# Performance work log

Hardware: AMD Instinct MI355X
Metric: run time of the kernel (lower is better)

## Reference

```python
import jax, jax.numpy as jnp
import numpy as np

EPS = 1e-5

def masked_group_norm(x, mask, gamma, beta, num_groups):
    # x: [B,D,H,W,C] (zero at unoccupied), mask: [B,D,H,W,1] float
    B, D, H, W, C = x.shape
    G = num_groups
    Cg = C // G
    xg = x.reshape(B, -1, G, Cg)          # [B,V,G,Cg]
    m = mask.reshape(B, -1, 1, 1)         # [B,V,1,1]
    cnt = jnp.maximum(m.sum(axis=1, keepdims=True) * Cg, 1.0)  # elems per (B,G)
    mean = (xg * m).sum(axis=(1, 3), keepdims=True) / cnt
    var = (((xg - mean) ** 2) * m).sum(axis=(1, 3), keepdims=True) / cnt
    y = (xg - mean) * jax.lax.rsqrt(var + EPS)
    y = y.reshape(B, D, H, W, C)
    return (y * gamma + beta) * mask

def downsample2(x, mask):
    # mean-pool occupied children under coords//2; new site occupied if any child is
    B, D, H, W, C = x.shape
    xr = x.reshape(B, D // 2, 2, H // 2, 2, W // 2, 2, C)
    mr = mask.reshape(B, D // 2, 2, H // 2, 2, W // 2, 2, 1)
    cnt = mr.sum(axis=(2, 4, 6))
    y = xr.sum(axis=(2, 4, 6)) / jnp.maximum(cnt, 1.0)
    new_mask = (cnt > 0).astype(x.dtype)
    return y, new_mask

def subm_conv3d(x, w, b, mask):
    # submanifold conv: unoccupied inputs are zero; outputs only at occupied sites
    y = jax.lax.conv_general_dilated(
        x, w, window_strides=(1, 1, 1), padding='SAME',
        dimension_numbers=('NDHWC', 'DHWIO', 'NDHWC'))
    return (y + b) * mask

def setup_inputs() -> dict:
    key = jax.random.key(0)
    ks = jax.random.split(key, 12)
    B, D, C, Co = 4, 64, 64, 128
    x = jax.random.normal(ks[0], (B, D, D, D, C), dtype=jnp.float32)
    mask = jax.random.randint(ks[1], (B, D, D, D), 0, 2).astype(jnp.int32)
    s = 0.05
    return {
        'x': x, 'mask': mask,
        'gn1_w': jnp.ones((C,), jnp.float32), 'gn1_b': jnp.zeros((C,), jnp.float32),
        'w1': jax.random.normal(ks[2], (3, 3, 3, C, Co), jnp.float32) * s,
        'b1': jax.random.normal(ks[3], (Co,), jnp.float32) * s,
        'gn2_w': jnp.ones((Co,), jnp.float32), 'gn2_b': jnp.zeros((Co,), jnp.float32),
        'w2': jax.random.normal(ks[4], (3, 3, 3, Co, Co), jnp.float32) * s,
        'b2': jax.random.normal(ks[5], (Co,), jnp.float32) * s,
        'wskip': jax.random.normal(ks[6], (C, Co), jnp.float32) * s,
        'bskip': jax.random.normal(ks[7], (Co,), jnp.float32) * s,
    }

def reference(x, mask, gn1_w, gn1_b, w1, b1, gn2_w, gn2_b, w2, b2, wskip, bskip):
    NUM_GROUPS = 32
    m = mask.astype(x.dtype)[..., None]          # [B,D,H,W,1]
    x = x * m                                    # sparse tensor: zero off-mask
    # act_layers: SparseGroupNorm32 + SparseSiLU
    h = masked_group_norm(x, m, gn1_w, gn1_b, NUM_GROUPS)
    h = jax.nn.silu(h)                           # silu(0)=0, stays sparse
    # downsample both h and residual x
    h, dm = downsample2(h, m)
    xd, _ = downsample2(x, m)
    # out_layers: conv3 -> GN -> SiLU -> conv3
    h = subm_conv3d(h, w1, b1, dm)
    h = masked_group_norm(h, dm, gn2_w, gn2_b, NUM_GROUPS)
    h = jax.nn.silu(h)
    h = subm_conv3d(h, w2, b2, dm)
    # skip: 1x1 sparse conv (out_channels != channels)
    skip = (jnp.einsum('bdhwc,co->bdhwo', xd, wskip) + bskip) * dm
    return h + skip
```

## Files before the change

### kernel.cpp

```cpp
#include <hip/hip_runtime.h>
#include <cstdint>
#include <cstddef>

#define B_ 4
#define V1 262144
#define C1 64
#define V2 32768
#define C2 128
#define TOTV 131072
#define P_ 34
#define P2_ 1156
#define P3_ 39304
#define SBSTRIDE ((size_t)4 * P3_)

#define OFF_S1A 0
#define OFF_S2A 128
#define OFF_CNT1 256
#define OFF_S1B 260
#define OFF_S2B 388
#define OFF_CNT2 516

typedef __bf16 bf16x8 __attribute__((ext_vector_type(8)));
typedef float f32x4 __attribute__((ext_vector_type(4)));

__device__ __forceinline__ float bf2f(unsigned short u) {
    return __builtin_bit_cast(float, (unsigned)u << 16);
}
__device__ __forceinline__ unsigned short f2bf(float f) {
    unsigned u = __builtin_bit_cast(unsigned, f);
    u += 0x7fffu + ((u >> 16) & 1u);
    return (unsigned short)(u >> 16);
}

__device__ __forceinline__ int a_ofs(int ks, int csh) {
    int s = ks & ((1 << csh) - 1), tap = ks >> csh;
    int dz = tap / 9, r = tap % 9, dy = r / 3, dx = r % 3;
    return s * (int)(SBSTRIDE * 64) + (dz * P2_ + dy * P_ + dx) * 64;
}

__global__ __launch_bounds__(256) void k0_wprep(const float* __restrict__ w1,
                                                const float* __restrict__ w2,
                                                const float* __restrict__ wskip,
                                                unsigned short* __restrict__ w1t,
                                                unsigned short* __restrict__ w2t,
                                                int* __restrict__ d1,
                                                int* __restrict__ d2)
{
    int i = blockIdx.x * 256 + threadIdx.x;
    if (blockIdx.x == 0) {
        int t = threadIdx.x;
        if (t < 54)               d1[t] = (t + 1 < 54)  ? a_ofs(t + 1, 1) - a_ofs(t, 1) : 0;
        if (t >= 64 && t < 172) { int j = t - 64;
                                  d2[j] = (j + 1 < 108) ? a_ofs(j + 1, 2) - a_ofs(j, 2) : 0; }
    }
    if (i < 54 * 4096) {
        int slab = i >> 12, r = i & 4095;
        int q = r >> 10, n = (r >> 3) & 127, j = r & 7;
        int t = slab >> 1, s = slab & 1;
        int ci = s * 32 + q * 8 + j;
        w1t[i] = f2bf(w1[((size_t)t * 64 + ci) * 128 + n]);
    }
    int i2 = i - 54 * 4096;
    if (i2 >= 0 && i2 < 110 * 4096) {
        int slab = i2 >> 12, r = i2 & 4095;
        int q = r >> 10, n = (r >> 3) & 127, j = r & 7;
        float v;
        if (slab < 108) {
            int t = slab >> 2, s = slab & 3;
            int ci = s * 32 + q * 8 + j;
            v = w2[((size_t)t * 128 + ci) * 128 + n];
        } else {
            int ci = (slab - 108) * 32 + q * 8 + j;
            v = wskip[(size_t)ci * 128 + n];
        }
        w2t[i2] = f2bf(v);
    }
}

__global__ __launch_bounds__(256) void kz_border(unsigned short* __restrict__ h1p,
                                                 unsigned short* __restrict__ h2p)
{
    int i = blockIdx.x * 256 + threadIdx.x;
    if (i >= 24 * P3_) return;
    int sb = i / P3_, vox = i % P3_;
    int vz = vox / P2_, r = vox % P2_, vy = r / P_, vx = r % P_;
    bool border = (vz == 0) | (vz == 33) | (vy == 0) | (vy == 33) | (vx == 0) | (vx == 33);
    if (!border) return;
    unsigned short* base = (sb < 8) ? (h1p + (size_t)sb * P3_ * 32 + (size_t)vox * 32)
                                    : (h2p + (size_t)(sb - 8) * P3_ * 32 + (size_t)vox * 32);
    uint4 z = {0, 0, 0, 0};
    uint4* b4 = (uint4*)base;
    b4[0] = z; b4[1] = z; b4[2] = z; b4[3] = z;
}

__global__ __launch_bounds__(256) void k1_stats1(const float* __restrict__ x,
                                                 const int* __restrict__ mask,
                                                 float* __restrict__ stats)
{
    __shared__ float ls1[32], ls2[32];
    __shared__ float lcnt;
    int tid = threadIdx.x;
    if (tid < 32) { ls1[tid] = 0.f; ls2[tid] = 0.f; }
    if (tid == 0) lcnt = 0.f;
    __syncthreads();

    int b  = blockIdx.x & 3;
    int bb = blockIdx.x >> 2;
    int c4 = tid & 15;
    int vl = tid >> 4;

    const float* xb = x + ((size_t)b * V1) * C1;
    const int*   mb = mask + (size_t)b * V1;

    float s1a = 0.f, s2a = 0.f, s1b = 0.f, s2b = 0.f, mc = 0.f;
    for (int ch = bb; ch < V1 / 16; ch += 1024) {
        int v = ch * 16 + vl;
        int m = mb[v];
        if (c4 == 0) mc += (float)m;
        if (m) {
            float4 xv = *(const float4*)(xb + (size_t)v * C1 + c4 * 4);
            s1a += xv.x + xv.y;  s2a += xv.x * xv.x + xv.y * xv.y;
            s1b += xv.z + xv.w;  s2b += xv.z * xv.z + xv.w * xv.w;
        }
    }
    atomicAdd(&ls1[2 * c4],     s1a); atomicAdd(&ls2[2 * c4],     s2a);
    atomicAdd(&ls1[2 * c4 + 1], s1b); atomicAdd(&ls2[2 * c4 + 1], s2b);
    if (c4 == 0) atomicAdd(&lcnt, mc);
    __syncthreads();
    if (tid < 32) {
        atomicAdd(&stats[OFF_S1A + b * 32 + tid], ls1[tid]);
        atomicAdd(&stats[OFF_S2A + b * 32 + tid], ls2[tid]);
    }
    if (tid == 0) atomicAdd(&stats[OFF_CNT1 + b], lcnt);
}

__global__ __launch_bounds__(256) void k2_down(const float* __restrict__ x,
                                               const int* __restrict__ mask,
                                               const float* __restrict__ gn1w,
                                               const float* __restrict__ gn1b,
                                               const float* __restrict__ stats,
                                               unsigned short* __restrict__ h1p,
                                               unsigned short* __restrict__ xdb,
                                               float* __restrict__ dm)
{
    int tid = threadIdx.x;
    int c  = tid & 63;
    int vl = tid >> 6;
    size_t ov = (size_t)blockIdx.x * 4 + vl;
    int b  = (int)(ov >> 15);
    int v2 = (int)(ov & 32767);
    int z = v2 >> 10, y = (v2 >> 5) & 31, xk = v2 & 31;

    int g = c >> 1;
    float ce   = fmaxf(stats[OFF_CNT1 + b] * 2.f, 1.f);
    float mean = stats[OFF_S1A + b * 32 + g] / ce;
    float var  = stats[OFF_S2A + b * 32 + g] / ce - mean * mean;
    float rinv = rsqrtf(var + 1e-5f);
    float a  = rinv * gn1w[c];
    float bc = gn1b[c] - mean * a;

    const int*   mb = mask + ((size_t)b << 18);
    const float* xb = x + (((size_t)b << 18) << 6);

    float hacc = 0.f, xacc = 0.f; int cnt = 0;
    #pragma unroll
    for (int dz = 0; dz < 2; ++dz)
    #pragma unroll
    for (int dy = 0; dy < 2; ++dy)
    #pragma unroll
    for (int dx = 0; dx < 2; ++dx) {
        int v1 = ((2 * z + dz) << 12) | ((2 * y + dy) << 6) | (2 * xk + dx);
        if (mb[v1]) {
            cnt++;
            float xv = xb[(size_t)v1 * 64 + c];
            xacc += xv;
            float yv = fmaf(xv, a, bc);
            hacc += yv / (1.f + expf(-yv));
        }
    }
    float inv = 1.f / fmaxf((float)cnt, 1.f);
    int pvox = (z + 1) * P2_ + (y + 1) * P_ + (xk + 1);
    size_t so = ((size_t)(c >> 5) * SBSTRIDE + (size_t)b * P3_ + pvox) * 32 + (c & 31);
    h1p[so] = f2bf(hacc * inv);
    xdb[ov * 64 + c] = f2bf(xacc * inv);
    if (c == 0) dm[ov] = (cnt > 0) ? 1.f : 0.f;
}

template<int CIN, bool SKIP>
__global__ __launch_bounds__(256, 4) void conv3_mfma(
    const unsigned short* __restrict__ srcP,
    const unsigned short* __restrict__ sksrc,
    const unsigned short* __restrict__ wT,
    const int* __restrict__ tblA,
    const float* __restrict__ bias,
    const float* __restrict__ bias2,
    const float* __restrict__ dm,
    float* __restrict__ outf,
    unsigned short* __restrict__ outb)
{
    constexpr int CS   = CIN / 32;
    constexpr int NKM  = 27 * CS;
    constexpr int NPHM = NKM / 2;
    constexpr int NPH  = NPHM + (SKIP ? 1 : 0);

    __shared__ short smem[2][8192];

    const int tid  = threadIdx.x;
    const int lane = tid & 63;
    const int wv   = tid >> 6;
    const int orig = blockIdx.x;
    const int blk  = (orig & 7) * 128 + (orig >> 3);
    const int b    = blk >> 8;
    const int z    = (blk >> 3) & 31;
    const int yo   = blk & 7;
    const int y0   = yo * 4 + wv;
    const int vb   = b * 32768;
    const int klo  = (lane >> 4) * 8;
    const int xl   = lane & 15;
    const int rlo  = (lane >> 4) * 4;

    f32x4 acc[2][8];
    #pragma unroll
    for (int f = 0; f < 2; ++f)
        #pragma unroll
        for (int nb = 0; nb < 8; ++nb)
            acc[f][nb] = (f32x4){0.f, 0.f, 0.f, 0.f};

    const char* pA = (const char*)srcP +
        (((size_t)b * P3_ + (size_t)(z * P2_ + y0 * P_ + xl)) * 32 + klo) * 2;

    auto loadSkip = [&](int ss, bf16x8* af) {
        const unsigned short* abase = sksrc + ss * 32;
        #pragma unroll
        for (int f = 0; f < 2; ++f) {
            int xx = f * 16 + xl;
            af[f] = *(const bf16x8*)(abase +
                     (size_t)(vb + z * 1024 + y0 * 32 + xx) * 64 + klo);
        }
    };

    auto stageW = [&](int pr, int buf) {
        const char* g = (const char*)wT + (size_t)pr * 16384 + wv * 1024 + (lane << 4);
        char* l = (char*)&smem[0][0] + buf * 16384 + wv * 1024;
        #pragma unroll
        for (int j = 0; j < 4; ++j)
            __builtin_amdgcn_global_load_lds(
                (const __attribute__((address_space(1))) unsigned int*)(g + j * 4096),
                (__attribute__((address_space(3))) unsigned int*)(l + j * 4096),
                16, 0, 0);
    };

    bf16x8 afc[4];
    stageW(0, 0);
    afc[0] = *(const bf16x8*)pA; afc[1] = *(const bf16x8*)(pA + 1024); pA += tblA[0];
    afc[2] = *(const bf16x8*)pA; afc[3] = *(const bf16x8*)(pA + 1024); pA += tblA[1];
    asm volatile("s_waitcnt vmcnt(4)" ::: "memory");
    __builtin_amdgcn_s_barrier();

    int cur = 0;
    #pragma unroll 2
    for (int p = 0; p < NPH; ++p) {
        const bool more = (p + 1 < NPH);
        bf16x8 afn[4] = {{}, {}, {}, {}};
        if (more) {
            stageW(p + 1, cur ^ 1);
            if (2 * p + 2 < NKM) {
                afn[0] = *(const bf16x8*)pA; afn[1] = *(const bf16x8*)(pA + 1024);
                pA += tblA[2 * p + 2];
                afn[2] = *(const bf16x8*)pA; afn[3] = *(const bf16x8*)(pA + 1024);
                pA += tblA[2 * p + 3];
            } else if (SKIP) {
                loadSkip(0, &afn[0]);
                loadSkip(1, &afn[2]);
            }
        }
        __builtin_amdgcn_s_setprio(1);
        #pragma unroll
        for (int ss = 0; ss < 2; ++ss) {
            const short* bp = &smem[0][0] + cur * 8192 + ss * 4096 +
                              ((lane >> 4) * 128 + xl) * 8;
            #pragma unroll
            for (int nb = 0; nb < 8; ++nb) {
                bf16x8 bfr = *(const bf16x8*)(bp + nb * 128);
                acc[0][nb] = __builtin_amdgcn_mfma_f32_16x16x32_bf16(afc[ss * 2 + 0], bfr, acc[0][nb], 0, 0, 0);
                acc[1][nb] = __builtin_amdgcn_mfma_f32_16x16x32_bf16(afc[ss * 2 + 1], bfr, acc[1][nb], 0, 0, 0);
            }
        }
        __builtin_amdgcn_s_setprio(0);
        if (more) asm volatile("s_waitcnt vmcnt(4)" ::: "memory");
        else      asm volatile("s_waitcnt vmcnt(0)" ::: "memory");
        asm volatile("s_waitcnt lgkmcnt(0)" ::: "memory");
        __builtin_amdgcn_s_barrier();
        afc[0] = afn[0]; afc[1] = afn[1]; afc[2] = afn[2]; afc[3] = afn[3];
        cur ^= 1;
    }

    float bv[8];
    #pragma unroll
    for (int nb = 0; nb < 8; ++nb) {
        int co = nb * 16 + xl;
        if constexpr (SKIP) bv[nb] = bias[co] + bias2[co];
        else                bv[nb] = bias[co];
    }
    #pragma unroll
    for (int f = 0; f < 2; ++f) {
        int xb2 = f * 16 + rlo;
        #pragma unroll
        for (int j = 0; j < 4; ++j) {
            int vox = vb + z * 1024 + y0 * 32 + xb2 + j;
            float dmx = dm[vox];
            #pragma unroll
            for (int nb = 0; nb < 8; ++nb) {
                float o = (acc[f][nb][j] + bv[nb]) * dmx;
                if constexpr (SKIP) outf[(size_t)vox * 128 + nb * 16 + xl] = o;
                else                outb[(size_t)vox * 128 + nb * 16 + xl] = f2bf(o);
            }
        }
    }
}

__global__ __launch_bounds__(256) void k4_stats2(const unsigned short* __restrict__ h2a,
                                                 const float* __restrict__ dm,
                                                 float* __restrict__ stats)
{
    __shared__ float ls1[32], ls2[32];
    __shared__ float lcnt;
    int tid = threadIdx.x;
    if (tid < 32) { ls1[tid] = 0.f; ls2[tid] = 0.f; }
    if (tid == 0) lcnt = 0.f;
    __syncthreads();

    int b  = blockIdx.x & 3;
    int bb = blockIdx.x >> 2;
    int g  = tid & 31;
    int vl = tid >> 5;

    const unsigned short* hb = h2a + ((size_t)b * V2) * C2;
    const float* dmb = dm + (size_t)b * V2;

    float s1 = 0.f, s2 = 0.f, mc = 0.f;
    for (int ch = bb; ch < V2 / 8; ch += 1024) {
        int v = ch * 8 + vl;
        float m = dmb[v];
        if (g == 0) mc += m;
        if (m != 0.f) {
            ushort4 hv = *(const ushort4*)(hb + (size_t)v * C2 + g * 4);
            float h0 = bf2f(hv.x), h1 = bf2f(hv.y), h2 = bf2f(hv.z), h3 = bf2f(hv.w);
            s1 += h0 + h1 + h2 + h3;
            s2 += h0 * h0 + h1 * h1 + h2 * h2 + h3 * h3;
        }
    }
    atomicAdd(&ls1[g], s1); atomicAdd(&ls2[g], s2);
    if (g == 0) atomicAdd(&lcnt, mc);
    __syncthreads();
    if (tid < 32) {
        atomicAdd(&stats[OFF_S1B + b * 32 + tid], ls1[tid]);
        atomicAdd(&stats[OFF_S2B + b * 32 + tid], ls2[tid]);
    }
    if (tid == 0) atomicAdd(&stats[OFF_CNT2 + b], lcnt);
}

__global__ __launch_bounds__(256) void k5_gn2(const unsigned short* __restrict__ h2a,
                                              unsigned short* __restrict__ h2p,
                                              const float* __restrict__ stats,
                                              const float* __restrict__ dm,
                                              const float* __restrict__ gn2w,
                                              const float* __restrict__ gn2b)
{
    int idx = blockIdx.x * 256 + threadIdx.x;
    int v = idx >> 5, g = idx & 31;
    int b = v >> 15;
    int v2 = v & 32767;
    float ce   = fmaxf(stats[OFF_CNT2 + b] * 4.f, 1.f);
    float mean = stats[OFF_S1B + b * 32 + g] / ce;
    float var  = stats[OFF_S2B + b * 32 + g] / ce - mean * mean;
    float rinv = rsqrtf(var + 1e-5f);
    float dmv  = dm[v];
    ushort4 hv = *(const ushort4*)(h2a + (size_t)idx * 4);
    float4 gw = *(const float4*)(gn2w + g * 4);
    float4 gb = *(const float4*)(gn2b + g * 4);
    float a, t;
    ushort4 o;
    a = rinv * gw.x; t = (fmaf(bf2f(hv.x), a, gb.x - mean * a)) * dmv; o.x = f2bf(t / (1.f + expf(-t)));
    a = rinv * gw.y; t = (fmaf(bf2f(hv.y), a, gb.y - mean * a)) * dmv; o.y = f2bf(t / (1.f + expf(-t)));
    a = rinv * gw.z; t = (fmaf(bf2f(hv.z), a, gb.z - mean * a)) * dmv; o.z = f2bf(t / (1.f + expf(-t)));
    a = rinv * gw.w; t = (fmaf(bf2f(hv.w), a, gb.w - mean * a)) * dmv; o.w = f2bf(t / (1.f + expf(-t)));
    int zz = v2 >> 10, yy = (v2 >> 5) & 31, xx = v2 & 31;
    int pvox = (zz + 1) * P2_ + (yy + 1) * P_ + (xx + 1);
    size_t so = ((size_t)(g >> 3) * SBSTRIDE + (size_t)b * P3_ + pvox) * 32 + (g & 7) * 4;
    *(ushort4*)(h2p + so) = o;
}

extern "C" void kernel_launch(void* const* d_in, const int* in_sizes, int n_in,
                              void* d_out, int out_size, void* d_ws, size_t ws_size,
                              hipStream_t stream)
{
    const float* x     = (const float*)d_in[0];
    const int*   mask  = (const int*)d_in[1];
    const float* gn1w  = (const float*)d_in[2];
    const float* gn1b  = (const float*)d_in[3];
    const float* w1    = (const float*)d_in[4];
    const float* b1    = (const float*)d_in[5];
    const float* gn2w  = (const float*)d_in[6];
    const float* gn2b  = (const float*)d_in[7];
    const float* w2    = (const float*)d_in[8];
    const float* b2    = (const float*)d_in[9];
    const float* wskip = (const float*)d_in[10];
    const float* bskip = (const float*)d_in[11];
    float* out = (float*)d_out;

    char* wsb = (char*)d_ws;
    float*          stats = (float*)wsb;
    float*          dm    = (float*)(wsb + 4096);
    unsigned short* h1p   = (unsigned short*)(wsb + 528384);
    unsigned short* xdb   = (unsigned short*)(wsb + 20652032);
    unsigned short* h2a   = (unsigned short*)(wsb + 37429248);
    unsigned short* h2p   = (unsigned short*)(wsb + 70983680);
    unsigned short* w1t   = (unsigned short*)(wsb + 111230976);
    unsigned short* w2t   = (unsigned short*)(wsb + 111673344);
    int*            d1    = (int*)(wsb + 112574464);
    int*            d2    = (int*)(wsb + 112574720);

    hipMemsetAsync(stats, 0, 520 * sizeof(float), stream);

    hipLaunchKernelGGL(k0_wprep, dim3(2624), dim3(256), 0, stream, w1, w2, wskip, w1t, w2t, d1, d2);
    hipLaunchKernelGGL(kz_border, dim3((24 * P3_ + 255) / 256), dim3(256), 0, stream, h1p, h2p);
    hipLaunchKernelGGL(k1_stats1, dim3(4096), dim3(256), 0, stream, x, mask, stats);
    hipLaunchKernelGGL(k2_down, dim3(32768), dim3(256), 0, stream,
                       x, mask, gn1w, gn1b, stats, h1p, xdb, dm);
    hipLaunchKernelGGL((conv3_mfma<64, false>), dim3(1024), dim3(256), 0, stream,
                       h1p, (const unsigned short*)nullptr, w1t, d1, b1, (const float*)nullptr,
                       dm, (float*)nullptr, h2a);
    hipLaunchKernelGGL(k4_stats2, dim3(4096), dim3(256), 0, stream, h2a, dm, stats);
    hipLaunchKernelGGL(k5_gn2, dim3(16384), dim3(256), 0, stream, h2a, h2p, stats, dm, gn2w, gn2b);
    hipLaunchKernelGGL((conv3_mfma<128, true>), dim3(1024), dim3(256), 0, stream,
                       h2p, xdb, w2t, d2, b2, bskip, dm, out, (unsigned short*)nullptr);
}
```

Baseline: 442.1 us.

## Double per-wave output tile in conv MFMA kernels to reuse weight fragments

Each wave now computes two y-rows (64 voxels) instead of one, holding 4x8 accumulators. Each LDS weight fragment then feeds four MFMAs instead of two, which halves LDS weight traffic and weight staging per output. The grid is halved to 512 blocks and launch bounds drop to 2 blocks per CU. In exchange, register pressure and A-fragment loads per step double, and occupancy falls, with only 512 blocks to spread over the GPU's CUs. The dm epilogue now loads four mask values at once with a float4.

```diff
diff --git a/kernel.cpp b/kernel.cpp
--- a/kernel.cpp
+++ b/kernel.cpp
@@ -187,7 +187,7 @@
 }
 
 template<int CIN, bool SKIP>
-__global__ __launch_bounds__(256, 4) void conv3_mfma(
+__global__ __launch_bounds__(256, 2) void conv3_mfma(
     const unsigned short* __restrict__ srcP,
     const unsigned short* __restrict__ sksrc,
     const unsigned short* __restrict__ wT,
@@ -209,19 +209,19 @@
     const int lane = tid & 63;
     const int wv   = tid >> 6;
     const int orig = blockIdx.x;
-    const int blk  = (orig & 7) * 128 + (orig >> 3);
-    const int b    = blk >> 8;
-    const int z    = (blk >> 3) & 31;
-    const int yo   = blk & 7;
-    const int y0   = yo * 4 + wv;
+    const int blk  = (orig & 7) * 64 + (orig >> 3);
+    const int b    = blk >> 7;
+    const int z    = (blk >> 2) & 31;
+    const int yo   = blk & 3;
+    const int y0   = yo * 8 + wv * 2;
     const int vb   = b * 32768;
     const int klo  = (lane >> 4) * 8;
     const int xl   = lane & 15;
     const int rlo  = (lane >> 4) * 4;
 
-    f32x4 acc[2][8];
-    #pragma unroll
-    for (int f = 0; f < 2; ++f)
+    f32x4 acc[4][8];
+    #pragma unroll
+    for (int f = 0; f < 4; ++f)
         #pragma unroll
         for (int nb = 0; nb < 8; ++nb)
             acc[f][nb] = (f32x4){0.f, 0.f, 0.f, 0.f};
@@ -232,11 +232,11 @@
     auto loadSkip = [&](int ss, bf16x8* af) {
         const unsigned short* abase = sksrc + ss * 32;
         #pragma unroll
-        for (int f = 0; f < 2; ++f) {
-            int xx = f * 16 + xl;
-            af[f] = *(const bf16x8*)(abase +
-                     (size_t)(vb + z * 1024 + y0 * 32 + xx) * 64 + klo);
-        }
+        for (int fy = 0; fy < 2; ++fy)
+            #pragma unroll
+            for (int fx = 0; fx < 2; ++fx)
+                af[fy * 2 + fx] = *(const bf16x8*)(abase +
+                    (size_t)(vb + z * 1024 + (y0 + fy) * 32 + fx * 16 + xl) * 64 + klo);
     };
 
     auto stageW = [&](int pr, int buf) {
@@ -250,28 +250,34 @@
                 16, 0, 0);
     };
 
-    bf16x8 afc[4];
+    auto loadAStep = [&](int ks, bf16x8* af) {
+        af[0] = *(const bf16x8*)pA;
+        af[1] = *(const bf16x8*)(pA + 1024);
+        af[2] = *(const bf16x8*)(pA + 2176);
+        af[3] = *(const bf16x8*)(pA + 3200);
+        pA += tblA[ks];
+    };
+
+    bf16x8 afc[8];
     stageW(0, 0);
-    afc[0] = *(const bf16x8*)pA; afc[1] = *(const bf16x8*)(pA + 1024); pA += tblA[0];
-    afc[2] = *(const bf16x8*)pA; afc[3] = *(const bf16x8*)(pA + 1024); pA += tblA[1];
-    asm volatile("s_waitcnt vmcnt(4)" ::: "memory");
+    loadAStep(0, &afc[0]);
+    loadAStep(1, &afc[4]);
+    asm volatile("s_waitcnt vmcnt(8)" ::: "memory");
     __builtin_amdgcn_s_barrier();
 
     int cur = 0;
     #pragma unroll 2
     for (int p = 0; p < NPH; ++p) {
         const bool more = (p + 1 < NPH);
-        bf16x8 afn[4] = {{}, {}, {}, {}};
+        bf16x8 afn[8] = {{}, {}, {}, {}, {}, {}, {}, {}};
         if (more) {
             stageW(p + 1, cur ^ 1);
             if (2 * p + 2 < NKM) {
-                afn[0] = *(const bf16x8*)pA; afn[1] = *(const bf16x8*)(pA + 1024);
-                pA += tblA[2 * p + 2];
-                afn[2] = *(const bf16x8*)pA; afn[3] = *(const bf16x8*)(pA + 1024);
-                pA += tblA[2 * p + 3];
+                loadAStep(2 * p + 2, &afn[0]);
+                loadAStep(2 * p + 3, &afn[4]);
             } else if (SKIP) {
                 loadSkip(0, &afn[0]);
-                loadSkip(1, &afn[2]);
+                loadSkip(1, &afn[4]);
             }
         }
         __builtin_amdgcn_s_setprio(1);
@@ -282,16 +288,19 @@
             #pragma unroll
             for (int nb = 0; nb < 8; ++nb) {
                 bf16x8 bfr = *(const bf16x8*)(bp + nb * 128);
-                acc[0][nb] = __builtin_amdgcn_mfma_f32_16x16x32_bf16(afc[ss * 2 + 0], bfr, acc[0][nb], 0, 0, 0);
-                acc[1][nb] = __builtin_amdgcn_mfma_f32_16x16x32_bf16(afc[ss * 2 + 1], bfr, acc[1][nb], 0, 0, 0);
+                acc[0][nb] = __builtin_amdgcn_mfma_f32_16x16x32_bf16(afc[ss * 4 + 0], bfr, acc[0][nb], 0, 0, 0);
+                acc[1][nb] = __builtin_amdgcn_mfma_f32_16x16x32_bf16(afc[ss * 4 + 1], bfr, acc[1][nb], 0, 0, 0);
+                acc[2][nb] = __builtin_amdgcn_mfma_f32_16x16x32_bf16(afc[ss * 4 + 2], bfr, acc[2][nb], 0, 0, 0);
+                acc[3][nb] = __builtin_amdgcn_mfma_f32_16x16x32_bf16(afc[ss * 4 + 3], bfr, acc[3][nb], 0, 0, 0);
             }
         }
         __builtin_amdgcn_s_setprio(0);
-        if (more) asm volatile("s_waitcnt vmcnt(4)" ::: "memory");
+        if (more) asm volatile("s_waitcnt vmcnt(8)" ::: "memory");
         else      asm volatile("s_waitcnt vmcnt(0)" ::: "memory");
         asm volatile("s_waitcnt lgkmcnt(0)" ::: "memory");
         __builtin_amdgcn_s_barrier();
-        afc[0] = afn[0]; afc[1] = afn[1]; afc[2] = afn[2]; afc[3] = afn[3];
+        #pragma unroll
+        for (int j = 0; j < 8; ++j) afc[j] = afn[j];
         cur ^= 1;
     }
 
@@ -303,17 +312,19 @@
         else                bv[nb] = bias[co];
     }
     #pragma unroll
-    for (int f = 0; f < 2; ++f) {
-        int xb2 = f * 16 + rlo;
+    for (int f = 0; f < 4; ++f) {
+        const int fy = f >> 1, fx = f & 1;
+        const int vox0 = vb + z * 1024 + (y0 + fy) * 32 + fx * 16 + rlo;
+        float4 dm4 = *(const float4*)(dm + vox0);
         #pragma unroll
         for (int j = 0; j < 4; ++j) {
-            int vox = vb + z * 1024 + y0 * 32 + xb2 + j;
-            float dmx = dm[vox];
+            const float dmx = (j == 0) ? dm4.x : (j == 1) ? dm4.y : (j == 2) ? dm4.z : dm4.w;
+            const size_t obase = (size_t)(vox0 + j) * 128 + xl;
             #pragma unroll
             for (int nb = 0; nb < 8; ++nb) {
                 float o = (acc[f][nb][j] + bv[nb]) * dmx;
-                if constexpr (SKIP) outf[(size_t)vox * 128 + nb * 16 + xl] = o;
-                else                outb[(size_t)vox * 128 + nb * 16 + xl] = f2bf(o);
+                if constexpr (SKIP) outf[obase + nb * 16] = o;
+                else                outb[obase + nb * 16] = f2bf(o);
             }
         }
     }
@@ -428,11 +439,11 @@
     hipLaunchKernelGGL(k1_stats1, dim3(4096), dim3(256), 0, stream, x, mask, stats);
     hipLaunchKernelGGL(k2_down, dim3(32768), dim3(256), 0, stream,
                        x, mask, gn1w, gn1b, stats, h1p, xdb, dm);
-    hipLaunchKernelGGL((conv3_mfma<64, false>), dim3(1024), dim3(256), 0, stream,
+    hipLaunchKernelGGL((conv3_mfma<64, false>), dim3(512), dim3(256), 0, stream,
                        h1p, (const unsigned short*)nullptr, w1t, d1, b1, (const float*)nullptr,
                        dm, (float*)nullptr, h2a);
     hipLaunchKernelGGL(k4_stats2, dim3(4096), dim3(256), 0, stream, h2a, dm, stats);
     hipLaunchKernelGGL(k5_gn2, dim3(16384), dim3(256), 0, stream, h2a, h2p, stats, dm, gn2w, gn2b);
-    hipLaunchKernelGGL((conv3_mfma<128, true>), dim3(1024), dim3(256), 0, stream,
+    hipLaunchKernelGGL((conv3_mfma<128, true>), dim3(512), dim3(256), 0, stream,
                        h2p, xdb, w2t, d2, b2, bskip, dm, out, (unsigned short*)nullptr);
 }
```

Measured after the change: 441.2 us. No clear change (-0.2%).
